# Kernel tuning notes

Hardware: AMD Instinct MI355X
Metric: run time of the kernel (lower is better)

The kernel has to match this reference:

```python
import jax, jax.numpy as jnp
import numpy as np

B, LQ, LK = 8, 1024, 1024
DQ, DK, DV = 1024, 1024, 1024
H = 16
DEPTH = DQ // H  # 64


def setup_inputs() -> dict:
    key = jax.random.key(0)
    ks = jax.random.split(key, 6)
    query = jax.random.normal(ks[0], (B, LQ, DQ), dtype=jnp.float32)
    keys = jax.random.normal(ks[1], (B, LK, DK), dtype=jnp.float32)
    values = jax.random.normal(ks[2], (B, LK, DV), dtype=jnp.float32)
    # Per-head Linear weights (torch Linear: y = x @ W.T, W is [depth, in_dim]);
    # stacked across heads -> [H, depth, in_dim].
    Wq = jax.random.normal(ks[3], (H, DEPTH, DQ), dtype=jnp.float32) / np.sqrt(DQ).astype(np.float32)
    Wk = jax.random.normal(ks[4], (H, DEPTH, DK), dtype=jnp.float32) / np.sqrt(DK).astype(np.float32)
    Wv = jax.random.normal(ks[5], (H, DEPTH, DV), dtype=jnp.float32) / np.sqrt(DV).astype(np.float32)
    return {"query": query, "keys": keys, "values": values, "Wq": Wq, "Wk": Wk, "Wv": Wv}


def reference(query, keys, values, Wq, Wk, Wv):
    depth = Wq.shape[1]
    # Fused per-head projections (replaces the Python loop of small GEMMs)
    q = jnp.einsum('bld,hed->bhle', query, Wq)   # [B,H,Lq,depth]
    k = jnp.einsum('bsd,hed->bhse', keys, Wk)    # [B,H,Lk,depth]
    v = jnp.einsum('bsd,hed->bhse', values, Wv)  # [B,H,Lk,depth]
    scale = jnp.asarray(1.0 / np.sqrt(depth), dtype=q.dtype)
    scores = jnp.einsum('bhle,bhse->bhls', q, k) * scale  # [B,H,Lq,Lk]
    weights = jax.nn.softmax(scores, axis=-1)
    out = jnp.einsum('bhls,bhse->bhle', weights, v)       # [B,H,Lq,depth]
    bsz = query.shape[0]
    # transpose(1,2) then flatten -> [B, Lq*H*depth]
    return out.transpose(0, 2, 1, 3).reshape(bsz, -1)
```

## Files before the change

### kernel.cpp

```cpp
#include <hip/hip_runtime.h>


typedef __attribute__((ext_vector_type(8))) short short8;
typedef __attribute__((ext_vector_type(4))) float f32x4;

typedef const void __attribute__((address_space(1)))* gas_cvptr;
typedef void __attribute__((address_space(3)))* las_vptr;

__device__ __forceinline__ void gll16(const void* g, void* l) {
  __builtin_amdgcn_global_load_lds((gas_cvptr)g, (las_vptr)l, 16, 0, 0);
}

__device__ __forceinline__ unsigned short f2bf(float f) {
  unsigned u = __builtin_bit_cast(unsigned, f);
  u += 0x7fffu + ((u >> 16) & 1u);
  return (unsigned short)(u >> 16);
}

__device__ __forceinline__ unsigned pack2bf(float a, float b) {
  unsigned ua = __builtin_bit_cast(unsigned, a) + 0x8000u;
  unsigned ub = __builtin_bit_cast(unsigned, b) + 0x8000u;
  return (ua >> 16) | (ub & 0xffff0000u);
}

__device__ __forceinline__ float fexp2(float x) {
#if __has_builtin(__builtin_amdgcn_exp2f)
  return __builtin_amdgcn_exp2f(x);
#else
  return exp2f(x);
#endif
}

#define SCALE_L2E 0.18033688011112042f
__global__ void cvt_all(const float* __restrict__ q, const float* __restrict__ k,
                        const float* __restrict__ v, const float* __restrict__ wq,
                        const float* __restrict__ wk, const float* __restrict__ wv,
                        unsigned short* __restrict__ out) {
  long e = ((long)blockIdx.x * 256 + threadIdx.x) * 8;
  const float* src;
  float scale = 1.0f;
  if (e < 25165824) {
    src = (e < 8388608) ? q + e : (e < 16777216) ? k + (e - 8388608) : v + (e - 16777216);
  } else if (e < 26214400) {
    src = wq + (e - 25165824); scale = SCALE_L2E;
  } else if (e < 27262976) {
    src = wk + (e - 26214400);
  } else {
    src = wv + (e - 27262976);
  }
  float4 a = ((const float4*)src)[0], b = ((const float4*)src)[1];
  short8 o;
  o[0] = (short)f2bf(a.x * scale); o[1] = (short)f2bf(a.y * scale);
  o[2] = (short)f2bf(a.z * scale); o[3] = (short)f2bf(a.w * scale);
  o[4] = (short)f2bf(b.x * scale); o[5] = (short)f2bf(b.y * scale);
  o[6] = (short)f2bf(b.z * scale); o[7] = (short)f2bf(b.w * scale);
  *(short8*)(out + e) = o;
}

__global__ __launch_bounds__(256, 2) void proj_gemm(
    const unsigned short* __restrict__ xq, const unsigned short* __restrict__ xk,
    const unsigned short* __restrict__ xv, const unsigned short* __restrict__ bwq,
    const unsigned short* __restrict__ bwk, const unsigned short* __restrict__ bwv,
    unsigned short* __restrict__ qp, unsigned short* __restrict__ kp,
    unsigned short* __restrict__ vpT) {
  __shared__ unsigned short sAB[2 * 128 * 64];
  unsigned short* sA = sAB;
  unsigned short* sB = sAB + 8192;

  const int z = blockIdx.z;
  const unsigned short* A  = z == 0 ? xq  : z == 1 ? xk  : xv;
  const unsigned short* Bt = z == 0 ? bwq : z == 1 ? bwk : bwv;
  unsigned short* Cp       = z == 0 ? qp  : z == 1 ? kp  : vpT;

  const int tid = threadIdx.x;
  const int lane = tid & 63, wv = tid >> 6;
  const int quad = lane >> 4, l16 = lane & 15;
  const int wm = wv >> 1, wn = wv & 1;
  const int m0 = blockIdx.y * 128, n0 = blockIdx.x * 128;
  const int key = l16 & 7;

  f32x4 acc[4][4];
  const f32x4 zero = {0.f, 0.f, 0.f, 0.f};
#pragma unroll
  for (int i = 0; i < 4; ++i)
#pragma unroll
    for (int j = 0; j < 4; ++j) acc[i][j] = zero;

  for (int kt = 0; kt < 16; ++kt) {
    const unsigned short* Ag = A + (size_t)m0 * 1024 + kt * 64;
    const unsigned short* Bg = Bt + (size_t)n0 * 1024 + kt * 64;
#pragma unroll
    for (int i = 0; i < 4; ++i) {
      int c = tid + i * 256;
      int row = c >> 3, cp = c & 7;
      int col = (cp ^ (row & 7)) * 8;
      gll16(Ag + (size_t)row * 1024 + col, (char*)sA + c * 16);
      gll16(Bg + (size_t)row * 1024 + col, (char*)sB + c * 16);
    }
    __syncthreads();
#pragma unroll
    for (int ks = 0; ks < 2; ++ks) {
      short8 af[4], bf[4];
      const int sw = ((ks * 4 + quad) ^ key) * 8;
#pragma unroll
      for (int t = 0; t < 4; ++t) {
        af[t] = *(const short8*)(sA + (wm * 64 + t * 16 + l16) * 64 + sw);
        bf[t] = *(const short8*)(sB + (wn * 64 + t * 16 + l16) * 64 + sw);
      }
#pragma unroll
      for (int mt = 0; mt < 4; ++mt)
#pragma unroll
        for (int nt = 0; nt < 4; ++nt)
          acc[mt][nt] = __builtin_amdgcn_mfma_f32_16x16x32_bf16(
              af[mt], bf[nt], acc[mt][nt], 0, 0, 0);
    }
    __syncthreads();
  }

  unsigned short* sC = sAB;
  const int h0 = blockIdx.x * 2;
  const int bb = m0 >> 10, l0 = m0 & 1023;
  if (z != 2) {
#pragma unroll
    for (int mt = 0; mt < 4; ++mt)
#pragma unroll
      for (int nt = 0; nt < 4; ++nt)
#pragma unroll
        for (int r = 0; r < 4; ++r)
          sC[wn * 8192 + (wm * 64 + mt * 16 + quad * 4 + r) * 64 + nt * 16 + l16] =
              f2bf(acc[mt][nt][r]);
    __syncthreads();
    const size_t base = (((size_t)(bb * 16 + h0)) * 1024 + l0) * 64;
#pragma unroll
    for (int i = 0; i < 8; ++i) {
      int ch = tid + i * 256;
      int hh = ch >> 10, inner = (ch & 1023) * 8;
      *(short8*)(Cp + base + (size_t)hh * 65536 + inner) =
          *(const short8*)(sC + hh * 8192 + inner);
    }
  } else {
#pragma unroll
    for (int mt = 0; mt < 4; ++mt)
#pragma unroll
      for (int nt = 0; nt < 4; ++nt)
#pragma unroll
        for (int r = 0; r < 4; ++r) {
          int rowIdx = wn * 64 + nt * 16 + l16;
          int l = wm * 64 + mt * 16 + quad * 4 + r;
          sC[rowIdx * 128 + (((l >> 3) ^ (rowIdx & 15)) << 3) + (l & 7)] =
              f2bf(acc[mt][nt][r]);
        }
    __syncthreads();
#pragma unroll
    for (int i = 0; i < 8; ++i) {
      int ch = tid + i * 256;
      int hh = ch >> 10, x = ch & 1023;
      int e = x >> 4, c = x & 15;
      int rowIdx = hh * 64 + e;
      short8 val = *(const short8*)(sC + rowIdx * 128 + ((c ^ (rowIdx & 15)) << 3));
      *(short8*)(Cp + ((size_t)(bb * 16 + h0 + hh) << 16) + (size_t)e * 1024 + l0 + c * 8) = val;
    }
  }
}

__global__ __launch_bounds__(256, 3) void attn(
    const unsigned short* __restrict__ qp,
    const unsigned short* __restrict__ kp,
    const unsigned short* __restrict__ vpT,
    float* __restrict__ out) {
  __shared__ unsigned short sQ[128 * 64];
  __shared__ unsigned short sK[64 * 64];
  __shared__ unsigned short sV[64 * 64];
  __shared__ unsigned short sP[4][32 * 64];

  const int tid = threadIdx.x;
  const int lane = tid & 63, wv = tid >> 6;
  const int quad = lane >> 4, l16 = lane & 15;
  const int bh = blockIdx.x;
  const int qt = blockIdx.y;
  const int b = bh >> 4, h = bh & 15;
  const int key = l16 & 7;

  const unsigned short* Qg = qp + ((size_t)bh * 1024 + qt * 128) * 64;
  const unsigned short* Kg = kp + (size_t)bh * 65536;
  const unsigned short* Vg = vpT + (size_t)bh * 65536;
  unsigned short* sPw = sP[wv];

#pragma unroll
  for (int i = 0; i < 4; ++i) {
    int c = tid + i * 256;
    int row = c >> 3, cp = c & 7;
    gll16(Qg + row * 64 + ((cp ^ (row & 7)) * 8), (char*)sQ + c * 16);
  }

  const f32x4 zero = {0.f, 0.f, 0.f, 0.f};
  f32x4 oaccT[4][2];
  float lsum[2] = {0.f, 0.f};
#pragma unroll
  for (int et = 0; et < 4; ++et)
#pragma unroll
    for (int qc = 0; qc < 2; ++qc) oaccT[et][qc] = zero;

  for (int kt = 0; kt < 16; ++kt) {
    __syncthreads();
#pragma unroll
    for (int i = 0; i < 2; ++i) {
      int c = tid + i * 256;
      int row = c >> 3, cp = c & 7;
      gll16(Kg + (size_t)kt * 4096 + row * 64 + ((cp ^ (row & 7)) * 8),
            (char*)sK + c * 16);
      gll16(Vg + (size_t)row * 1024 + kt * 64 + ((cp ^ (row & 7)) * 8),
            (char*)sV + c * 16);
    }
    __syncthreads();

    f32x4 sacc[4][2];
#pragma unroll
    for (int st = 0; st < 4; ++st)
#pragma unroll
      for (int qc = 0; qc < 2; ++qc) sacc[st][qc] = zero;
#pragma unroll
    for (int ks = 0; ks < 2; ++ks) {
      short8 kf[4], qf[2];
      const int sw = ((ks * 4 + quad) ^ key) * 8;
#pragma unroll
      for (int st = 0; st < 4; ++st)
        kf[st] = *(const short8*)(sK + (st * 16 + l16) * 64 + sw);
#pragma unroll
      for (int qc = 0; qc < 2; ++qc)
        qf[qc] = *(const short8*)(sQ + (wv * 32 + qc * 16 + l16) * 64 + sw);
#pragma unroll
      for (int st = 0; st < 4; ++st)
#pragma unroll
        for (int qc = 0; qc < 2; ++qc)
          sacc[st][qc] = __builtin_amdgcn_mfma_f32_16x16x32_bf16(
              kf[st], qf[qc], sacc[st][qc], 0, 0, 0);
    }

#pragma unroll
    for (int st = 0; st < 4; ++st)
#pragma unroll
      for (int qc = 0; qc < 2; ++qc) {
        float p0 = fexp2(sacc[st][qc][0]);
        float p1 = fexp2(sacc[st][qc][1]);
        float p2 = fexp2(sacc[st][qc][2]);
        float p3 = fexp2(sacc[st][qc][3]);
        lsum[qc] += (p0 + p1) + (p2 + p3);
        uint2 pk;
        pk.x = pack2bf(p0, p1);
        pk.y = pack2bf(p2, p3);
        int up = (st * 4 + quad) ^ (key << 1);
        *(uint2*)(sPw + (qc * 16 + l16) * 64 + up * 4) = pk;
      }

#pragma unroll
    for (int ks = 0; ks < 2; ++ks) {
      short8 vf[4], pf[2];
      const int sw = ((ks * 4 + quad) ^ key) * 8;
      const int swp = ((ks * 8 + quad * 2) ^ (key << 1)) * 4;
#pragma unroll
      for (int et = 0; et < 4; ++et)
        vf[et] = *(const short8*)(sV + (et * 16 + l16) * 64 + sw);
#pragma unroll
      for (int qc = 0; qc < 2; ++qc)
        pf[qc] = *(const short8*)(sPw + (qc * 16 + l16) * 64 + swp);
#pragma unroll
      for (int et = 0; et < 4; ++et)
#pragma unroll
        for (int qc = 0; qc < 2; ++qc)
          oaccT[et][qc] = __builtin_amdgcn_mfma_f32_16x16x32_bf16(
              vf[et], pf[qc], oaccT[et][qc], 0, 0, 0);
    }
  }

  float inv[2];
#pragma unroll
  for (int qc = 0; qc < 2; ++qc) {
    float l = lsum[qc];
    l += __shfl_xor(l, 16);
    l += __shfl_xor(l, 32);
    inv[qc] = 1.0f / l;
  }

#pragma unroll
  for (int et = 0; et < 4; ++et)
#pragma unroll
    for (int qc = 0; qc < 2; ++qc) {
      int qg = qt * 128 + wv * 32 + qc * 16 + l16;
      int e0 = et * 16 + quad * 4;
      float4 o;
      o.x = oaccT[et][qc][0] * inv[qc];
      o.y = oaccT[et][qc][1] * inv[qc];
      o.z = oaccT[et][qc][2] * inv[qc];
      o.w = oaccT[et][qc][3] * inv[qc];
      *(float4*)(out + ((size_t)b << 20) + (size_t)qg * 1024 + h * 64 + e0) = o;
    }
}

extern "C" void kernel_launch(void* const* d_in, const int* in_sizes, int n_in,
                              void* d_out, int out_size, void* d_ws, size_t ws_size,
                              hipStream_t stream) {
  const float* q  = (const float*)d_in[0];
  const float* k  = (const float*)d_in[1];
  const float* v  = (const float*)d_in[2];
  const float* wq = (const float*)d_in[3];
  const float* wk = (const float*)d_in[4];
  const float* wv = (const float*)d_in[5];
  float* out = (float*)d_out;

  const size_t E = (size_t)8 * 1024 * 1024;
  const size_t W = (size_t)16 * 64 * 1024;
  const size_t need = (6 * E + 3 * W) * sizeof(unsigned short);
  if (ws_size < need) return;

  unsigned short* ws  = (unsigned short*)d_ws;
  unsigned short* xq  = ws;
  unsigned short* xk  = ws + E;
  unsigned short* xv  = ws + 2 * E;
  unsigned short* bwq = ws + 3 * E;
  unsigned short* bwk = ws + 3 * E + W;
  unsigned short* bwv = ws + 3 * E + 2 * W;
  unsigned short* qp  = ws + 3 * E + 3 * W;
  unsigned short* kp  = qp + E;
  unsigned short* vpT = qp + 2 * E;

  cvt_all<<<dim3((unsigned)((3 * E + 3 * W) / 2048)), 256, 0, stream>>>(
      q, k, v, wq, wk, wv, ws);

  proj_gemm<<<dim3(8, 64, 3), 256, 0, stream>>>(xq, xk, xv, bwq, bwk, bwv,
                                                qp, kp, vpT);

  attn<<<dim3(128, 8), 256, 0, stream>>>(qp, kp, vpT, out);
}
```

Before: 276.7 us.

## Fuse activation bf16 conversion into projection GEMM, remap grid, enlarge attention Q tile

The standalone conversion of the fp32 activations is removed. The projection GEMM now loads fp32 A tiles directly and converts them to bf16 into LDS with round-to-nearest-even, so the bf16 copies of q, k and v are never written to or read back from global memory. The projection grid becomes a flat 1D launch with an XCD-aware block remapping. The attention kernel processes 256 queries per block instead of 128, keeps Q fragments in registers for the whole KV loop, and lowers occupancy to 2 blocks per SM, so each K/V tile is reused across more queries. The costs are synchronous global loads in the GEMM A path in place of async LDS loads, and higher register pressure in attention.

```diff
diff --git a/kernel.cpp b/kernel.cpp
--- a/kernel.cpp
+++ b/kernel.cpp
@@ -15,6 +15,10 @@
   unsigned u = __builtin_bit_cast(unsigned, f);
   u += 0x7fffu + ((u >> 16) & 1u);
   return (unsigned short)(u >> 16);
+}
+
+__device__ __forceinline__ unsigned pack2bf_rne(float lo, float hi) {
+  return (unsigned)f2bf(lo) | ((unsigned)f2bf(hi) << 16);
 }
 
 __device__ __forceinline__ unsigned pack2bf(float a, float b) {
@@ -32,22 +36,14 @@
 }
 
 #define SCALE_L2E 0.18033688011112042f
-__global__ void cvt_all(const float* __restrict__ q, const float* __restrict__ k,
-                        const float* __restrict__ v, const float* __restrict__ wq,
-                        const float* __restrict__ wk, const float* __restrict__ wv,
-                        unsigned short* __restrict__ out) {
+__global__ void cvt_w(const float* __restrict__ wq, const float* __restrict__ wk,
+                      const float* __restrict__ wv, unsigned short* __restrict__ out) {
   long e = ((long)blockIdx.x * 256 + threadIdx.x) * 8;
   const float* src;
   float scale = 1.0f;
-  if (e < 25165824) {
-    src = (e < 8388608) ? q + e : (e < 16777216) ? k + (e - 8388608) : v + (e - 16777216);
-  } else if (e < 26214400) {
-    src = wq + (e - 25165824); scale = SCALE_L2E;
-  } else if (e < 27262976) {
-    src = wk + (e - 26214400);
-  } else {
-    src = wv + (e - 27262976);
-  }
+  if (e < 1048576) { src = wq + e; scale = SCALE_L2E; }
+  else if (e < 2097152) src = wk + (e - 1048576);
+  else src = wv + (e - 2097152);
   float4 a = ((const float4*)src)[0], b = ((const float4*)src)[1];
   short8 o;
   o[0] = (short)f2bf(a.x * scale); o[1] = (short)f2bf(a.y * scale);
@@ -58,25 +54,28 @@
 }
 
 __global__ __launch_bounds__(256, 2) void proj_gemm(
-    const unsigned short* __restrict__ xq, const unsigned short* __restrict__ xk,
-    const unsigned short* __restrict__ xv, const unsigned short* __restrict__ bwq,
-    const unsigned short* __restrict__ bwk, const unsigned short* __restrict__ bwv,
+    const float* __restrict__ aq, const float* __restrict__ ak,
+    const float* __restrict__ av, const unsigned short* __restrict__ bw,
     unsigned short* __restrict__ qp, unsigned short* __restrict__ kp,
     unsigned short* __restrict__ vpT) {
   __shared__ unsigned short sAB[2 * 128 * 64];
   unsigned short* sA = sAB;
   unsigned short* sB = sAB + 8192;
 
-  const int z = blockIdx.z;
-  const unsigned short* A  = z == 0 ? xq  : z == 1 ? xk  : xv;
-  const unsigned short* Bt = z == 0 ? bwq : z == 1 ? bwk : bwv;
-  unsigned short* Cp       = z == 0 ? qp  : z == 1 ? kp  : vpT;
+  const int id = blockIdx.x;
+  const int xcd = id & 7, kk = id >> 3;
+  const int x = kk & 7, j = kk >> 3;
+  const int yz = j * 8 + xcd;
+  const int z = yz >> 6, y = yz & 63;
+  const float* A = z == 0 ? aq : z == 1 ? ak : av;
+  const unsigned short* Bt = bw + (size_t)z * 1048576;
+  unsigned short* Cp = z == 0 ? qp : z == 1 ? kp : vpT;
 
   const int tid = threadIdx.x;
   const int lane = tid & 63, wv = tid >> 6;
   const int quad = lane >> 4, l16 = lane & 15;
   const int wm = wv >> 1, wn = wv & 1;
-  const int m0 = blockIdx.y * 128, n0 = blockIdx.x * 128;
+  const int m0 = y * 128, n0 = x * 128;
   const int key = l16 & 7;
 
   f32x4 acc[4][4];
@@ -84,18 +83,30 @@
 #pragma unroll
   for (int i = 0; i < 4; ++i)
 #pragma unroll
-    for (int j = 0; j < 4; ++j) acc[i][j] = zero;
+    for (int jj = 0; jj < 4; ++jj) acc[i][jj] = zero;
 
   for (int kt = 0; kt < 16; ++kt) {
-    const unsigned short* Ag = A + (size_t)m0 * 1024 + kt * 64;
+    const float* Ag = A + (size_t)m0 * 1024 + kt * 64;
     const unsigned short* Bg = Bt + (size_t)n0 * 1024 + kt * 64;
+#pragma unroll
+    for (int i = 0; i < 4; ++i) {
+      int c = tid + i * 256;
+      int row = c >> 3, cp = c & 7;
+      gll16(Bg + (size_t)row * 1024 + (cp ^ (row & 7)) * 8, (char*)sB + c * 16);
+    }
 #pragma unroll
     for (int i = 0; i < 4; ++i) {
       int c = tid + i * 256;
       int row = c >> 3, cp = c & 7;
       int col = (cp ^ (row & 7)) * 8;
-      gll16(Ag + (size_t)row * 1024 + col, (char*)sA + c * 16);
-      gll16(Bg + (size_t)row * 1024 + col, (char*)sB + c * 16);
+      const float* p = Ag + (size_t)row * 1024 + col;
+      float4 a = ((const float4*)p)[0], b = ((const float4*)p)[1];
+      uint4 o;
+      o.x = pack2bf_rne(a.x, a.y);
+      o.y = pack2bf_rne(a.z, a.w);
+      o.z = pack2bf_rne(b.x, b.y);
+      o.w = pack2bf_rne(b.z, b.w);
+      *(uint4*)((char*)sA + c * 16) = o;
     }
     __syncthreads();
 #pragma unroll
@@ -118,7 +129,7 @@
   }
 
   unsigned short* sC = sAB;
-  const int h0 = blockIdx.x * 2;
+  const int h0 = x * 2;
   const int bb = m0 >> 10, l0 = m0 & 1023;
   if (z != 2) {
 #pragma unroll
@@ -154,8 +165,8 @@
 #pragma unroll
     for (int i = 0; i < 8; ++i) {
       int ch = tid + i * 256;
-      int hh = ch >> 10, x = ch & 1023;
-      int e = x >> 4, c = x & 15;
+      int hh = ch >> 10, xx = ch & 1023;
+      int e = xx >> 4, c = xx & 15;
       int rowIdx = hh * 64 + e;
       short8 val = *(const short8*)(sC + rowIdx * 128 + ((c ^ (rowIdx & 15)) << 3));
       *(short8*)(Cp + ((size_t)(bb * 16 + h0 + hh) << 16) + (size_t)e * 1024 + l0 + c * 8) = val;
@@ -163,43 +174,52 @@
   }
 }
 
-__global__ __launch_bounds__(256, 3) void attn(
+__global__ __launch_bounds__(256, 2) void attn(
     const unsigned short* __restrict__ qp,
     const unsigned short* __restrict__ kp,
     const unsigned short* __restrict__ vpT,
     float* __restrict__ out) {
-  __shared__ unsigned short sQ[128 * 64];
+  __shared__ unsigned short sQ[256 * 64];
   __shared__ unsigned short sK[64 * 64];
   __shared__ unsigned short sV[64 * 64];
-  __shared__ unsigned short sP[4][32 * 64];
+  __shared__ unsigned short sP[4][64 * 64];
 
   const int tid = threadIdx.x;
   const int lane = tid & 63, wv = tid >> 6;
   const int quad = lane >> 4, l16 = lane & 15;
-  const int bh = blockIdx.x;
-  const int qt = blockIdx.y;
+  const int bh = blockIdx.x, qt = blockIdx.y;
   const int b = bh >> 4, h = bh & 15;
   const int key = l16 & 7;
 
-  const unsigned short* Qg = qp + ((size_t)bh * 1024 + qt * 128) * 64;
+  const unsigned short* Qg = qp + ((size_t)bh * 1024 + qt * 256) * 64;
   const unsigned short* Kg = kp + (size_t)bh * 65536;
   const unsigned short* Vg = vpT + (size_t)bh * 65536;
   unsigned short* sPw = sP[wv];
 
 #pragma unroll
-  for (int i = 0; i < 4; ++i) {
+  for (int i = 0; i < 8; ++i) {
     int c = tid + i * 256;
     int row = c >> 3, cp = c & 7;
-    gll16(Qg + row * 64 + ((cp ^ (row & 7)) * 8), (char*)sQ + c * 16);
+    gll16(Qg + row * 64 + (cp ^ (row & 7)) * 8, (char*)sQ + c * 16);
+  }
+  __syncthreads();
+
+  short8 qfr[2][4];
+#pragma unroll
+  for (int ks = 0; ks < 2; ++ks) {
+    const int sw = ((ks * 4 + quad) ^ key) * 8;
+#pragma unroll
+    for (int qc = 0; qc < 4; ++qc)
+      qfr[ks][qc] = *(const short8*)(sQ + (wv * 64 + qc * 16 + l16) * 64 + sw);
   }
 
   const f32x4 zero = {0.f, 0.f, 0.f, 0.f};
-  f32x4 oaccT[4][2];
-  float lsum[2] = {0.f, 0.f};
+  f32x4 oaccT[4][4];
+  float lsum[4] = {0.f, 0.f, 0.f, 0.f};
 #pragma unroll
   for (int et = 0; et < 4; ++et)
 #pragma unroll
-    for (int qc = 0; qc < 2; ++qc) oaccT[et][qc] = zero;
+    for (int qc = 0; qc < 4; ++qc) oaccT[et][qc] = zero;
 
   for (int kt = 0; kt < 16; ++kt) {
     __syncthreads();
@@ -207,40 +227,37 @@
     for (int i = 0; i < 2; ++i) {
       int c = tid + i * 256;
       int row = c >> 3, cp = c & 7;
-      gll16(Kg + (size_t)kt * 4096 + row * 64 + ((cp ^ (row & 7)) * 8),
+      gll16(Kg + (size_t)kt * 4096 + row * 64 + (cp ^ (row & 7)) * 8,
             (char*)sK + c * 16);
-      gll16(Vg + (size_t)row * 1024 + kt * 64 + ((cp ^ (row & 7)) * 8),
+      gll16(Vg + (size_t)row * 1024 + kt * 64 + (cp ^ (row & 7)) * 8,
             (char*)sV + c * 16);
     }
     __syncthreads();
 
-    f32x4 sacc[4][2];
+    f32x4 sacc[4][4];
 #pragma unroll
     for (int st = 0; st < 4; ++st)
 #pragma unroll
-      for (int qc = 0; qc < 2; ++qc) sacc[st][qc] = zero;
+      for (int qc = 0; qc < 4; ++qc) sacc[st][qc] = zero;
 #pragma unroll
     for (int ks = 0; ks < 2; ++ks) {
-      short8 kf[4], qf[2];
+      short8 kfr[4];
       const int sw = ((ks * 4 + quad) ^ key) * 8;
 #pragma unroll
       for (int st = 0; st < 4; ++st)
-        kf[st] = *(const short8*)(sK + (st * 16 + l16) * 64 + sw);
-#pragma unroll
-      for (int qc = 0; qc < 2; ++qc)
-        qf[qc] = *(const short8*)(sQ + (wv * 32 + qc * 16 + l16) * 64 + sw);
+        kfr[st] = *(const short8*)(sK + (st * 16 + l16) * 64 + sw);
 #pragma unroll
       for (int st = 0; st < 4; ++st)
 #pragma unroll
-        for (int qc = 0; qc < 2; ++qc)
+        for (int qc = 0; qc < 4; ++qc)
           sacc[st][qc] = __builtin_amdgcn_mfma_f32_16x16x32_bf16(
-              kf[st], qf[qc], sacc[st][qc], 0, 0, 0);
+              kfr[st], qfr[ks][qc], sacc[st][qc], 0, 0, 0);
     }
 
 #pragma unroll
     for (int st = 0; st < 4; ++st)
 #pragma unroll
-      for (int qc = 0; qc < 2; ++qc) {
+      for (int qc = 0; qc < 4; ++qc) {
         float p0 = fexp2(sacc[st][qc][0]);
         float p1 = fexp2(sacc[st][qc][1]);
         float p2 = fexp2(sacc[st][qc][2]);
@@ -255,27 +272,27 @@
 
 #pragma unroll
     for (int ks = 0; ks < 2; ++ks) {
-      short8 vf[4], pf[2];
+      short8 vfr[4], pfr[4];
       const int sw = ((ks * 4 + quad) ^ key) * 8;
       const int swp = ((ks * 8 + quad * 2) ^ (key << 1)) * 4;
 #pragma unroll
       for (int et = 0; et < 4; ++et)
-        vf[et] = *(const short8*)(sV + (et * 16 + l16) * 64 + sw);
-#pragma unroll
-      for (int qc = 0; qc < 2; ++qc)
-        pf[qc] = *(const short8*)(sPw + (qc * 16 + l16) * 64 + swp);
+        vfr[et] = *(const short8*)(sV + (et * 16 + l16) * 64 + sw);
+#pragma unroll
+      for (int qc = 0; qc < 4; ++qc)
+        pfr[qc] = *(const short8*)(sPw + (qc * 16 + l16) * 64 + swp);
 #pragma unroll
       for (int et = 0; et < 4; ++et)
 #pragma unroll
-        for (int qc = 0; qc < 2; ++qc)
+        for (int qc = 0; qc < 4; ++qc)
           oaccT[et][qc] = __builtin_amdgcn_mfma_f32_16x16x32_bf16(
-              vf[et], pf[qc], oaccT[et][qc], 0, 0, 0);
-    }
-  }
-
-  float inv[2];
-#pragma unroll
-  for (int qc = 0; qc < 2; ++qc) {
+              vfr[et], pfr[qc], oaccT[et][qc], 0, 0, 0);
+    }
+  }
+
+  float inv[4];
+#pragma unroll
+  for (int qc = 0; qc < 4; ++qc) {
     float l = lsum[qc];
     l += __shfl_xor(l, 16);
     l += __shfl_xor(l, 32);
@@ -285,8 +302,8 @@
 #pragma unroll
   for (int et = 0; et < 4; ++et)
 #pragma unroll
-    for (int qc = 0; qc < 2; ++qc) {
-      int qg = qt * 128 + wv * 32 + qc * 16 + l16;
+    for (int qc = 0; qc < 4; ++qc) {
+      int qg = qt * 256 + wv * 64 + qc * 16 + l16;
       int e0 = et * 16 + quad * 4;
       float4 o;
       o.x = oaccT[et][qc][0] * inv[qc];
@@ -310,25 +327,16 @@
 
   const size_t E = (size_t)8 * 1024 * 1024;
   const size_t W = (size_t)16 * 64 * 1024;
-  const size_t need = (6 * E + 3 * W) * sizeof(unsigned short);
+  const size_t need = (3 * E + 3 * W) * sizeof(unsigned short);
   if (ws_size < need) return;
 
   unsigned short* ws  = (unsigned short*)d_ws;
-  unsigned short* xq  = ws;
-  unsigned short* xk  = ws + E;
-  unsigned short* xv  = ws + 2 * E;
-  unsigned short* bwq = ws + 3 * E;
-  unsigned short* bwk = ws + 3 * E + W;
-  unsigned short* bwv = ws + 3 * E + 2 * W;
-  unsigned short* qp  = ws + 3 * E + 3 * W;
+  unsigned short* bw  = ws;
+  unsigned short* qp  = ws + 3 * W;
   unsigned short* kp  = qp + E;
   unsigned short* vpT = qp + 2 * E;
 
-  cvt_all<<<dim3((unsigned)((3 * E + 3 * W) / 2048)), 256, 0, stream>>>(
-      q, k, v, wq, wk, wv, ws);
-
-  proj_gemm<<<dim3(8, 64, 3), 256, 0, stream>>>(xq, xk, xv, bwq, bwk, bwv,
-                                                qp, kp, vpT);
-
-  attn<<<dim3(128, 8), 256, 0, stream>>>(qp, kp, vpT, out);
-}
+  cvt_w<<<dim3(1536), 256, 0, stream>>>(wq, wk, wv, bw);
+  proj_gemm<<<dim3(1536), 256, 0, stream>>>(q, k, v, bw, qp, kp, vpT);
+  attn<<<dim3(128, 4), 256, 0, stream>>>(qp, kp, vpT, out);
+}
```

After: 260.1 us. 6.0% less time.
